# Kernel optimization log

Hardware: AMD Instinct MI355X
Metric: run time of the kernel (lower is better)

Reference implementation:

```python
import jax, jax.numpy as jnp
import numpy as np

B, S, D = 2, 2048, 2048
N_HEADS = 16
HEAD_DIM = D // N_HEADS  # 128


def apply_rotary(xq, xk, cos, sin):
    # xq, xk: [B, S, H, HD]; cos, sin: [S, HD//2]
    def rot(t):
        tr = t.reshape(t.shape[:-1] + (HEAD_DIM // 2, 2))
        r, i = tr[..., 0], tr[..., 1]
        c = cos[None, :, None, :]  # [1, S, 1, HD//2]
        s = sin[None, :, None, :]
        out_r = r * c - i * s
        out_i = r * s + i * c
        return jnp.stack([out_r, out_i], axis=-1).reshape(t.shape)
    return rot(xq), rot(xk)


def setup_inputs() -> dict:
    key = jax.random.key(0)
    k1, k2, k3 = jax.random.split(key, 3)
    x = jax.random.normal(k1, (B, S, D), dtype=jnp.float32)
    wqkv = jax.random.normal(k2, (3 * D, D), dtype=jnp.float32) * (D ** -0.5)
    wo = jax.random.normal(k3, (D, D), dtype=jnp.float32) * (D ** -0.5)
    # rotary tables, standard llama theta=10000
    inv_freq = 1.0 / (10000.0 ** (jnp.arange(0, HEAD_DIM, 2, dtype=jnp.float32) / HEAD_DIM))
    t = jnp.arange(S, dtype=jnp.float32)
    freqs = jnp.outer(t, inv_freq)  # [S, HD//2]
    freqs_cos = jnp.cos(freqs)
    freqs_sin = jnp.sin(freqs)
    # causal additive mask [1, 1, S, S]
    causal = jnp.tril(jnp.ones((S, S), dtype=bool))
    mask = jnp.where(causal, 0.0, -jnp.inf).astype(jnp.float32)[None, None]
    return {"x": x, "freqs_cos": freqs_cos, "freqs_sin": freqs_sin,
            "mask": mask, "wqkv": wqkv, "wo": wo, "input_pos": 0}


def reference(x, freqs_cos, freqs_sin, mask, wqkv, wo, input_pos):
    # fused QKV projection (Linear: x @ W^T)
    qkv = jnp.einsum('bsd,ed->bse', x, wqkv)  # [B, S, 3D]
    xq, xk, xv = jnp.split(qkv, 3, axis=-1)
    xq = xq.reshape(B, S, N_HEADS, HEAD_DIM)
    xk = xk.reshape(B, S, N_HEADS, HEAD_DIM)
    xv = xv.reshape(B, S, N_HEADS, HEAD_DIM)
    xq, xk = apply_rotary(xq, xk, freqs_cos, freqs_sin)
    # SDPA (kv_cache is None; input_pos unused)
    scale = HEAD_DIM ** -0.5
    scores = jnp.einsum('bqhd,bkhd->bhqk', xq, xk) * scale + mask
    attn = jax.nn.softmax(scores, axis=-1)
    out = jnp.einsum('bhqk,bkhd->bqhd', attn, xv).reshape(B, S, D)
    return jnp.einsum('bsd,ed->bse', out, wo)
```

## Files before the change

### kernel.cpp

```cpp
#include <hip/hip_runtime.h>

#define B_ 2
#define S_ 2048
#define D_ 2048
#define H_ 16
#define DH_ 128
#define E3_ (3*D_)

#define AS1 __attribute__((address_space(1)))
#define AS3 __attribute__((address_space(3)))

typedef __attribute__((ext_vector_type(4))) float f32x4;
typedef __attribute__((ext_vector_type(8))) short bf16x8;

__device__ __forceinline__ unsigned short f2bf(float f) {
  unsigned u = __float_as_uint(f);
  u += 0x7fff + ((u >> 16) & 1);
  return (unsigned short)(u >> 16);
}
__device__ __forceinline__ float bf2f(unsigned short h) {
  return __uint_as_float(((unsigned)h) << 16);
}
__device__ __forceinline__ unsigned cvt_pk_bf16(float lo, float hi) {
  unsigned r;
  asm("v_cvt_pk_bf16_f32 %0, %1, %2" : "=v"(r) : "v"(lo), "v"(hi));
  return r;
}

__global__ void cast_f32_bf16(const float* __restrict__ in, unsigned short* __restrict__ out, int n4) {
  int i = blockIdx.x * 256 + threadIdx.x;
  if (i >= n4) return;
  float4 v = reinterpret_cast<const float4*>(in)[i];
  ushort4 o;
  o.x = f2bf(v.x); o.y = f2bf(v.y); o.z = f2bf(v.z); o.w = f2bf(v.w);
  reinterpret_cast<ushort4*>(out)[i] = o;
}

__global__ __launch_bounds__(512) void gemm_qkv256(const unsigned short* __restrict__ A,
                                                   const unsigned short* __restrict__ Bm,
                                                   unsigned short* __restrict__ qkv,
                                                   unsigned short* __restrict__ Vt) {
  __shared__ __align__(16) unsigned short As[2][256*64];
  __shared__ __align__(16) unsigned short Bs[2][192*64];
  const int t = threadIdx.x;
  const int lane = t & 63;
  const int w = t >> 6;
  const int wr = w >> 2, wc = w & 3;
  const int l16 = lane & 15, lg = lane >> 4;
  const int bm = blockIdx.y, bn = blockIdx.x;

  f32x4 acc[8][3] = {};

#define STG1(KT)                                                                                   \
  {                                                                                                \
    const int k0s = (KT) * 64;                                                                     \
    const int bufs = (KT) & 1;                                                                     \
    _Pragma("unroll")                                                                              \
    for (int rr = 0; rr < 4; ++rr) {                                                               \
      int e = t*8 + rr*4096;                                                                       \
      int row = e >> 6, g = (e >> 3) & 7, gs = g ^ (row & 7);                                      \
      const unsigned short* ga = A + (size_t)(bm*256 + row)*2048 + k0s + gs*8;                     \
      __builtin_amdgcn_global_load_lds((const AS1 unsigned int*)ga,                                \
                                       (AS3 unsigned int*)(&As[bufs][e]), 16, 0, 0);               \
    }                                                                                              \
    _Pragma("unroll")                                                                              \
    for (int rr = 0; rr < 3; ++rr) {                                                               \
      int e = t*8 + rr*4096;                                                                       \
      int row = e >> 6, g = (e >> 3) & 7, gs = g ^ (row & 7);                                      \
      const unsigned short* gb = Bm + (size_t)(bn*192 + row)*2048 + k0s + gs*8;                    \
      __builtin_amdgcn_global_load_lds((const AS1 unsigned int*)gb,                                \
                                       (AS3 unsigned int*)(&Bs[bufs][e]), 16, 0, 0);               \
    }                                                                                              \
  }

  STG1(0);
  STG1(1);

  for (int kt = 0; kt < 32; ++kt) {
    if (kt == 31) { asm volatile("s_waitcnt vmcnt(0)" ::: "memory"); }
    else         { asm volatile("s_waitcnt vmcnt(7)" ::: "memory"); }
    __builtin_amdgcn_s_barrier();
    __builtin_amdgcn_sched_barrier(0);
    const int buf = kt & 1;
#pragma unroll
    for (int kk = 0; kk < 2; ++kk) {
      bf16x8 bfr[3];
#pragma unroll
      for (int ni = 0; ni < 3; ++ni) {
        int row = wc*48 + ni*16 + l16;
        int g = kk*4 + lg;
        bfr[ni] = *reinterpret_cast<const bf16x8*>(&Bs[buf][row*64 + ((g ^ (row & 7))<<3)]);
      }
#pragma unroll
      for (int mh = 0; mh < 2; ++mh) {
        bf16x8 afr[4];
#pragma unroll
        for (int m4 = 0; m4 < 4; ++m4) {
          int row = wr*128 + (mh*4 + m4)*16 + l16;
          int g = kk*4 + lg;
          afr[m4] = *reinterpret_cast<const bf16x8*>(&As[buf][row*64 + ((g ^ (row & 7))<<3)]);
        }
#pragma unroll
        for (int m4 = 0; m4 < 4; ++m4)
#pragma unroll
          for (int ni = 0; ni < 3; ++ni)
            acc[mh*4 + m4][ni] = __builtin_amdgcn_mfma_f32_16x16x32_bf16(afr[m4], bfr[ni], acc[mh*4 + m4][ni], 0, 0, 0);
      }
    }
    __builtin_amdgcn_s_barrier();
    if (kt < 30) STG1(kt + 2);
  }
#undef STG1

#pragma unroll
  for (int mi = 0; mi < 8; ++mi) {
#pragma unroll
    for (int ni = 0; ni < 3; ++ni) {
      int col = bn*192 + wc*48 + ni*16 + l16;
      int row0 = bm*256 + wr*128 + mi*16 + lg*4;
      if (col < 4096) {
#pragma unroll
        for (int r = 0; r < 4; ++r)
          qkv[(size_t)(row0 + r)*4096 + col] = f2bf(acc[mi][ni][r]);
      } else {
        int colv = col - 4096;
        int h = colv >> 7, d = colv & 127;
        int b = row0 >> 11, s = row0 & 2047;
        ushort4 v4;
        v4.x = f2bf(acc[mi][ni][0]);
        v4.y = f2bf(acc[mi][ni][1]);
        v4.z = f2bf(acc[mi][ni][2]);
        v4.w = f2bf(acc[mi][ni][3]);
        *reinterpret_cast<ushort4*>(&Vt[(((size_t)(b*H_ + h))*DH_ + d)*S_ + s]) = v4;
      }
    }
  }
}

__global__ __launch_bounds__(256) void gemm_bt(const unsigned short* __restrict__ A,
                                               const unsigned short* __restrict__ Bm,
                                               float* __restrict__ C,
                                               int Ndim, int Kdim) {
  __shared__ __align__(16) unsigned short As[128*64];
  __shared__ __align__(16) unsigned short Bs[128*64];
  const int t = threadIdx.x;
  const int lane = t & 63;
  const int w = t >> 6;
  const int wm = w >> 1, wn = w & 1;
  const int l16 = lane & 15, lg = lane >> 4;
  const int bm = blockIdx.y, bn = blockIdx.x;

  f32x4 acc[4][4] = {};
  const int e0 = t * 8;

  for (int k0 = 0; k0 < Kdim; k0 += 64) {
#pragma unroll
    for (int it = 0; it < 4; ++it) {
      int e = e0 + it * 2048;
      int row = e >> 6;
      int g = (e >> 3) & 7;
      int gs = g ^ (row & 7);
      const unsigned short* ga = A  + (size_t)(bm*128 + row) * Kdim + k0 + gs*8;
      const unsigned short* gb = Bm + (size_t)(bn*128 + row) * Kdim + k0 + gs*8;
      __builtin_amdgcn_global_load_lds((const AS1 unsigned int*)ga,
                                       (AS3 unsigned int*)(&As[e]), 16, 0, 0);
      __builtin_amdgcn_global_load_lds((const AS1 unsigned int*)gb,
                                       (AS3 unsigned int*)(&Bs[e]), 16, 0, 0);
    }
    __syncthreads();
#pragma unroll
    for (int kk = 0; kk < 2; ++kk) {
      bf16x8 a[4], b[4];
#pragma unroll
      for (int mi = 0; mi < 4; ++mi) {
        int row = wm*64 + mi*16 + l16;
        int gw = kk*4 + lg;
        a[mi] = *reinterpret_cast<const bf16x8*>(&As[row*64 + ((gw ^ (row & 7))<<3)]);
      }
#pragma unroll
      for (int ni = 0; ni < 4; ++ni) {
        int row = wn*64 + ni*16 + l16;
        int gw = kk*4 + lg;
        b[ni] = *reinterpret_cast<const bf16x8*>(&Bs[row*64 + ((gw ^ (row & 7))<<3)]);
      }
#pragma unroll
      for (int mi = 0; mi < 4; ++mi)
#pragma unroll
        for (int ni = 0; ni < 4; ++ni)
          acc[mi][ni] = __builtin_amdgcn_mfma_f32_16x16x32_bf16(a[mi], b[ni], acc[mi][ni], 0, 0, 0);
    }
    __syncthreads();
  }
#pragma unroll
  for (int mi = 0; mi < 4; ++mi) {
#pragma unroll
    for (int ni = 0; ni < 4; ++ni) {
      int col = bn*128 + wn*64 + ni*16 + l16;
      int row0 = bm*128 + wm*64 + mi*16 + lg*4;
#pragma unroll
      for (int r = 0; r < 4; ++r)
        C[(size_t)(row0 + r) * Ndim + col] = acc[mi][ni][r];
    }
  }
}

__global__ __launch_bounds__(256) void rope_qk(const unsigned short* __restrict__ qkv,
                                               const float* __restrict__ cosT,
                                               const float* __restrict__ sinT,
                                               unsigned short* __restrict__ Q,
                                               unsigned short* __restrict__ K) {
  const float SCLQ = 0.08838834764831845f * 1.4426950408889634f;
  const int idx = blockIdx.x;
  const int b = idx >> 11, s = idx & 2047;
  const int t = threadIdx.x;
  const int e = t * 8;
  const int h = e >> 7, d0 = e & 127;
  const int j0 = d0 >> 1;
  const size_t rowb = (size_t)(b*S_ + s) * 4096;
  float4 c4 = *reinterpret_cast<const float4*>(&cosT[s*64 + j0]);
  float4 s4 = *reinterpret_cast<const float4*>(&sinT[s*64 + j0]);
  float cc[4] = {c4.x, c4.y, c4.z, c4.w};
  float ss[4] = {s4.x, s4.y, s4.z, s4.w};
  const size_t qo = (((size_t)(b*H_ + h)) * S_ + s) * DH_ + d0;

  ushort4 qv[2], kv[2], qd[2], kd[2];
  qv[0] = *reinterpret_cast<const ushort4*>(&qkv[rowb + e]);
  qv[1] = *reinterpret_cast<const ushort4*>(&qkv[rowb + e + 4]);
  kv[0] = *reinterpret_cast<const ushort4*>(&qkv[rowb + 2048 + e]);
  kv[1] = *reinterpret_cast<const ushort4*>(&qkv[rowb + 2048 + e + 4]);
#pragma unroll
  for (int p = 0; p < 4; ++p) {
    unsigned short* qi = (unsigned short*)&qv[p >> 1] + (p & 1) * 2;
    unsigned short* ki = (unsigned short*)&kv[p >> 1] + (p & 1) * 2;
    unsigned short* qo2 = (unsigned short*)&qd[p >> 1] + (p & 1) * 2;
    unsigned short* ko2 = (unsigned short*)&kd[p >> 1] + (p & 1) * 2;
    float x0 = bf2f(qi[0]), x1 = bf2f(qi[1]);
    qo2[0] = f2bf((x0*cc[p] - x1*ss[p]) * SCLQ);
    qo2[1] = f2bf((x0*ss[p] + x1*cc[p]) * SCLQ);
    float y0 = bf2f(ki[0]), y1 = bf2f(ki[1]);
    ko2[0] = f2bf(y0*cc[p] - y1*ss[p]);
    ko2[1] = f2bf(y0*ss[p] + y1*cc[p]);
  }
  *reinterpret_cast<ushort4*>(&Q[qo])     = qd[0];
  *reinterpret_cast<ushort4*>(&Q[qo + 4]) = qd[1];
  *reinterpret_cast<ushort4*>(&K[qo])     = kd[0];
  *reinterpret_cast<ushort4*>(&K[qo + 4]) = kd[1];
}

#define NQT 32
__global__ __launch_bounds__(512) void attn(const unsigned short* __restrict__ Q,
                                            const unsigned short* __restrict__ K,
                                            const unsigned short* __restrict__ Vt,
                                            unsigned short* __restrict__ O) {
  __shared__ __align__(16) unsigned short Ks[2][64*128];
  __shared__ __align__(16) unsigned short Vs[2][128*64];
  __shared__ __align__(16) unsigned short Plds[8][16*64];
  const int orig = blockIdx.y * gridDim.x + blockIdx.x;
  const int wgid = (orig & 7) * 64 + (orig >> 3);
  const int x = wgid & 15;
  const int bh = wgid >> 4;
  const int b = bh >> 4, h = bh & 15;
  const int t = threadIdx.x;
  const int lane = t & 63;
  const int w = t >> 6;
  const int wg8 = w >> 2;
  const int wi = w & 3;
  const int l16 = lane & 15, lg = lane >> 4;
  const int qt = wg8 ? (NQT - 1 - x) : x;
  const int q0 = qt * 64 + wi * 16;
  const unsigned short* Qh = Q  + (size_t)bh * S_ * DH_;
  const unsigned short* Kh = K  + (size_t)bh * S_ * DH_;
  const unsigned short* Vh = Vt + (size_t)bh * DH_ * S_;

  bf16x8 aq[4];
#pragma unroll
  for (int kk = 0; kk < 4; ++kk)
    aq[kk] = *reinterpret_cast<const bf16x8*>(Qh + (size_t)(q0 + l16)*DH_ + kk*32 + lg*8);

  f32x4 o[8] = {};
  float mrun = -1e30f, lrun = 0.f;
  const int ntiles = NQT - x;

#define STAGE_KV(TILE)                                                                              \
  {                                                                                                 \
    const int kv0s = (TILE) * 64;                                                                   \
    unsigned short* Kd = &Ks[(TILE) & 1][0];                                                        \
    unsigned short* Vd = &Vs[(TILE) & 1][0];                                                        \
    _Pragma("unroll")                                                                               \
    for (int it = 0; it < 2; ++it) {                                                                \
      int e = t*8 + it*4096;                                                                        \
      int row = e >> 7;                                                                             \
      int gslot = (e >> 3) & 15;                                                                    \
      int gsrc = gslot ^ (row & 7);                                                                 \
      const unsigned short* ga = Kh + (size_t)(kv0s + row) * DH_ + gsrc*8;                          \
      __builtin_amdgcn_global_load_lds((const AS1 unsigned int*)ga,                                 \
                                       (AS3 unsigned int*)(&Kd[e]), 16, 0, 0);                      \
    }                                                                                               \
    _Pragma("unroll")                                                                               \
    for (int it = 0; it < 2; ++it) {                                                                \
      int e = t*8 + it*4096;                                                                        \
      int dd = e >> 6;                                                                              \
      int gslot = (e >> 3) & 7;                                                                     \
      int gsrc = gslot ^ (dd & 7);                                                                  \
      const unsigned short* gv = Vh + (size_t)dd * S_ + kv0s + gsrc*8;                              \
      __builtin_amdgcn_global_load_lds((const AS1 unsigned int*)gv,                                 \
                                       (AS3 unsigned int*)(&Vd[e]), 16, 0, 0);                      \
    }                                                                                               \
  }

  STAGE_KV(0);

  for (int tile = 0; tile < ntiles; ++tile) {
    __syncthreads();
    if (tile + 1 < ntiles) STAGE_KV(tile + 1);
    const int kv0 = tile * 64;
    const int buf = tile & 1;

    if (tile <= qt) {
      f32x4 sc[4] = {};
      __builtin_amdgcn_s_setprio(1);
#pragma unroll
      for (int kk = 0; kk < 4; ++kk) {
#pragma unroll
        for (int n = 0; n < 4; ++n) {
          int row = n*16 + l16;
          int g = kk*4 + lg;
          bf16x8 bk = *reinterpret_cast<const bf16x8*>(&Ks[buf][row*128 + ((g ^ (row & 7))<<3)]);
          sc[n] = __builtin_amdgcn_mfma_f32_16x16x32_bf16(bk, aq[kk], sc[n], 0, 0, 0);
        }
      }
      __builtin_amdgcn_s_setprio(0);
      if (tile == qt) {
        int qrow = q0 + l16;
#pragma unroll
        for (int n = 0; n < 4; ++n)
#pragma unroll
          for (int r = 0; r < 4; ++r) {
            int kidx = kv0 + n*16 + lg*4 + r;
            sc[n][r] = (kidx > qrow) ? -1e30f : sc[n][r];
          }
      }
      float mt = sc[0][0];
#pragma unroll
      for (int n = 0; n < 4; ++n)
#pragma unroll
        for (int r = 0; r < 4; ++r) mt = fmaxf(mt, sc[n][r]);
      mt = fmaxf(mt, __shfl_xor(mt, 16));
      mt = fmaxf(mt, __shfl_xor(mt, 32));
      if (__any(mt > mrun + 8.f)) {
        float mnew = fmaxf(mrun, mt);
        float alpha = __builtin_amdgcn_exp2f(mrun - mnew);
        mrun = mnew;
        lrun *= alpha;
        float ar[4];
#pragma unroll
        for (int r = 0; r < 4; ++r) ar[r] = __shfl(alpha, lg*4 + r);
#pragma unroll
        for (int n2 = 0; n2 < 8; ++n2)
#pragma unroll
          for (int r = 0; r < 4; ++r) o[n2][r] *= ar[r];
      }
      float rs = 0.f;
      unsigned pk[4][2];
#pragma unroll
      for (int n = 0; n < 4; ++n) {
        float p0 = __builtin_amdgcn_exp2f(sc[n][0] - mrun);
        float p1 = __builtin_amdgcn_exp2f(sc[n][1] - mrun);
        float p2 = __builtin_amdgcn_exp2f(sc[n][2] - mrun);
        float p3 = __builtin_amdgcn_exp2f(sc[n][3] - mrun);
        rs += (p0 + p1) + (p2 + p3);
        pk[n][0] = cvt_pk_bf16(p0, p1);
        pk[n][1] = cvt_pk_bf16(p2, p3);
      }
      rs += __shfl_xor(rs, 16);
      rs += __shfl_xor(rs, 32);
      lrun += rs;
      unsigned short* Pw = &Plds[w][0];
      char* Pb = (char*)Pw + l16*128;
#pragma unroll
      for (int n = 0; n < 4; ++n) {
        int sslot = (n*4 + lg) ^ (l16 & 14);
        *reinterpret_cast<uint2*>(Pb + sslot*8) = make_uint2(pk[n][0], pk[n][1]);
      }
      bf16x8 pa[2];
#pragma unroll
      for (int kk2 = 0; kk2 < 2; ++kk2) {
        int tp = (kk2*4 + lg) ^ ((l16 >> 1) & 7);
        pa[kk2] = *reinterpret_cast<const bf16x8*>(Pb + tp*16);
      }
      __builtin_amdgcn_s_setprio(1);
#pragma unroll
      for (int kk2 = 0; kk2 < 2; ++kk2) {
#pragma unroll
        for (int n2 = 0; n2 < 8; ++n2) {
          int d = n2*16 + l16;
          int g = kk2*4 + lg;
          bf16x8 bv = *reinterpret_cast<const bf16x8*>(&Vs[buf][d*64 + ((g ^ (d & 7))<<3)]);
          o[n2] = __builtin_amdgcn_mfma_f32_16x16x32_bf16(pa[kk2], bv, o[n2], 0, 0, 0);
        }
      }
      __builtin_amdgcn_s_setprio(0);
    }
  }
  float linv = 1.f / lrun;
  float lr[4];
#pragma unroll
  for (int r = 0; r < 4; ++r) lr[r] = __shfl(linv, lg*4 + r);
  size_t ob = ((size_t)b * S_) * D_;
#pragma unroll
  for (int n2 = 0; n2 < 8; ++n2) {
#pragma unroll
    for (int r = 0; r < 4; ++r) {
      int rowq = q0 + lg*4 + r;
      int d = n2*16 + l16;
      O[ob + (size_t)rowq * D_ + h*DH_ + d] = f2bf(o[n2][r] * lr[r]);
    }
  }
}

extern "C" void kernel_launch(void* const* d_in, const int* in_sizes, int n_in,
                              void* d_out, int out_size, void* d_ws, size_t ws_size,
                              hipStream_t stream) {
  const float* x    = (const float*)d_in[0];
  const float* fcos = (const float*)d_in[1];
  const float* fsin = (const float*)d_in[2];
  const float* wqkv = (const float*)d_in[4];
  const float* wo   = (const float*)d_in[5];
  float* out = (float*)d_out;
  char* ws = (char*)d_ws;

  unsigned short* xb    = (unsigned short*)(ws);
  unsigned short* wqkvb = (unsigned short*)(ws + 16777216);
  unsigned short* wob   = (unsigned short*)(ws + 41943040);
  unsigned short* qkv   = (unsigned short*)(ws + 50331648);
  unsigned short* Qb    = (unsigned short*)(ws + 83886080);
  unsigned short* Kb    = (unsigned short*)(ws + 100663296);
  unsigned short* Vtb   = (unsigned short*)(ws + 117440512);
  unsigned short* attn_out = xb;

  cast_f32_bf16<<<dim3(2097152/256), 256, 0, stream>>>(x, xb, 2097152);
  cast_f32_bf16<<<dim3(3145728/256), 256, 0, stream>>>(wqkv, wqkvb, 3145728);
  cast_f32_bf16<<<dim3(1048576/256), 256, 0, stream>>>(wo, wob, 1048576);

  gemm_qkv256<<<dim3(32, 16), 512, 0, stream>>>(xb, wqkvb, qkv, Vtb);
  rope_qk<<<dim3(4096), 256, 0, stream>>>(qkv, fcos, fsin, Qb, Kb);
  attn<<<dim3(16, 32), 512, 0, stream>>>(Qb, Kb, Vtb, attn_out);
  gemm_bt<<<dim3(16, 32), 256, 0, stream>>>(attn_out, wob, out, 2048, 2048);
}
```

Measured before the change: 248.4 us.

## Double-buffer output GEMM, restructure QKV GEMM LDS reads, merge cast kernels

Merges the three fp32→bf16 cast launches into one kernel that picks its source by global index, removing two launches. Restructures the QKV GEMM inner loop so both k-halves of the fragments are read from LDS up front, with MFMA issue interleaved around the barrier and next-stage prefetch and wrapped in s_setprio. Converts the output-projection GEMM from single-buffered LDS with full syncthreads to a double-buffered global_load_lds pipeline with the same split-phase schedule. This doubles LDS use in gemm_bt and raises register pressure from holding both fragment halves, which may lower occupancy.

```diff
diff --git a/kernel.cpp b/kernel.cpp
--- a/kernel.cpp
+++ b/kernel.cpp
@@ -5,7 +5,6 @@
 #define D_ 2048
 #define H_ 16
 #define DH_ 128
-#define E3_ (3*D_)
 
 #define AS1 __attribute__((address_space(1)))
 #define AS3 __attribute__((address_space(3)))
@@ -27,13 +26,21 @@
   return r;
 }
 
-__global__ void cast_f32_bf16(const float* __restrict__ in, unsigned short* __restrict__ out, int n4) {
+__global__ __launch_bounds__(256) void cast3(const float* __restrict__ x,
+                                             const float* __restrict__ wq,
+                                             const float* __restrict__ wo,
+                                             unsigned short* __restrict__ xb,
+                                             unsigned short* __restrict__ wqb,
+                                             unsigned short* __restrict__ wob) {
   int i = blockIdx.x * 256 + threadIdx.x;
-  if (i >= n4) return;
-  float4 v = reinterpret_cast<const float4*>(in)[i];
+  const float* src; unsigned short* dst; int off;
+  if (i < 2097152)      { src = x;  dst = xb;  off = i; }
+  else if (i < 5242880) { src = wq; dst = wqb; off = i - 2097152; }
+  else                  { src = wo; dst = wob; off = i - 5242880; }
+  float4 v = reinterpret_cast<const float4*>(src)[off];
   ushort4 o;
   o.x = f2bf(v.x); o.y = f2bf(v.y); o.z = f2bf(v.z); o.w = f2bf(v.w);
-  reinterpret_cast<ushort4*>(out)[i] = o;
+  reinterpret_cast<ushort4*>(dst)[off] = o;
 }
 
 __global__ __launch_bounds__(512) void gemm_qkv256(const unsigned short* __restrict__ A,
@@ -77,38 +84,56 @@
   STG1(1);
 
   for (int kt = 0; kt < 32; ++kt) {
+    const int buf = kt & 1;
     if (kt == 31) { asm volatile("s_waitcnt vmcnt(0)" ::: "memory"); }
-    else         { asm volatile("s_waitcnt vmcnt(7)" ::: "memory"); }
+    else          { asm volatile("s_waitcnt vmcnt(7)" ::: "memory"); }
     __builtin_amdgcn_s_barrier();
     __builtin_amdgcn_sched_barrier(0);
-    const int buf = kt & 1;
-#pragma unroll
-    for (int kk = 0; kk < 2; ++kk) {
-      bf16x8 bfr[3];
-#pragma unroll
-      for (int ni = 0; ni < 3; ++ni) {
-        int row = wc*48 + ni*16 + l16;
-        int g = kk*4 + lg;
-        bfr[ni] = *reinterpret_cast<const bf16x8*>(&Bs[buf][row*64 + ((g ^ (row & 7))<<3)]);
-      }
-#pragma unroll
-      for (int mh = 0; mh < 2; ++mh) {
-        bf16x8 afr[4];
-#pragma unroll
-        for (int m4 = 0; m4 < 4; ++m4) {
-          int row = wr*128 + (mh*4 + m4)*16 + l16;
-          int g = kk*4 + lg;
-          afr[m4] = *reinterpret_cast<const bf16x8*>(&As[buf][row*64 + ((g ^ (row & 7))<<3)]);
-        }
-#pragma unroll
-        for (int m4 = 0; m4 < 4; ++m4)
-#pragma unroll
-          for (int ni = 0; ni < 3; ++ni)
-            acc[mh*4 + m4][ni] = __builtin_amdgcn_mfma_f32_16x16x32_bf16(afr[m4], bfr[ni], acc[mh*4 + m4][ni], 0, 0, 0);
-      }
-    }
+    bf16x8 a0[8], b0[3];
+#pragma unroll
+    for (int ni = 0; ni < 3; ++ni) {
+      int row = wc*48 + ni*16 + l16;
+      b0[ni] = *reinterpret_cast<const bf16x8*>(&Bs[buf][row*64 + ((lg ^ (row & 7))<<3)]);
+    }
+#pragma unroll
+    for (int m8 = 0; m8 < 8; ++m8) {
+      int row = wr*128 + m8*16 + l16;
+      a0[m8] = *reinterpret_cast<const bf16x8*>(&As[buf][row*64 + ((lg ^ (row & 7))<<3)]);
+    }
+    asm volatile("s_waitcnt lgkmcnt(0)" ::: "memory");
+    __builtin_amdgcn_sched_barrier(0);
+    bf16x8 a1[8], b1[3];
+#pragma unroll
+    for (int ni = 0; ni < 3; ++ni) {
+      int row = wc*48 + ni*16 + l16;
+      int g = 4 + lg;
+      b1[ni] = *reinterpret_cast<const bf16x8*>(&Bs[buf][row*64 + ((g ^ (row & 7))<<3)]);
+    }
+#pragma unroll
+    for (int m8 = 0; m8 < 8; ++m8) {
+      int row = wr*128 + m8*16 + l16;
+      int g = 4 + lg;
+      a1[m8] = *reinterpret_cast<const bf16x8*>(&As[buf][row*64 + ((g ^ (row & 7))<<3)]);
+    }
+    __builtin_amdgcn_sched_barrier(0);
+    __builtin_amdgcn_s_setprio(1);
+#pragma unroll
+    for (int m8 = 0; m8 < 8; ++m8)
+#pragma unroll
+      for (int ni = 0; ni < 3; ++ni)
+        acc[m8][ni] = __builtin_amdgcn_mfma_f32_16x16x32_bf16(a0[m8], b0[ni], acc[m8][ni], 0, 0, 0);
+    __builtin_amdgcn_s_setprio(0);
+    asm volatile("s_waitcnt lgkmcnt(0)" ::: "memory");
+    __builtin_amdgcn_sched_barrier(0);
     __builtin_amdgcn_s_barrier();
     if (kt < 30) STG1(kt + 2);
+    __builtin_amdgcn_s_setprio(1);
+#pragma unroll
+    for (int m8 = 0; m8 < 8; ++m8)
+#pragma unroll
+      for (int ni = 0; ni < 3; ++ni)
+        acc[m8][ni] = __builtin_amdgcn_mfma_f32_16x16x32_bf16(a1[m8], b1[ni], acc[m8][ni], 0, 0, 0);
+    __builtin_amdgcn_s_setprio(0);
   }
 #undef STG1
 
@@ -141,56 +166,85 @@
                                                const unsigned short* __restrict__ Bm,
                                                float* __restrict__ C,
                                                int Ndim, int Kdim) {
-  __shared__ __align__(16) unsigned short As[128*64];
-  __shared__ __align__(16) unsigned short Bs[128*64];
+  __shared__ __align__(16) unsigned short As[2][128*64];
+  __shared__ __align__(16) unsigned short Bs[2][128*64];
   const int t = threadIdx.x;
   const int lane = t & 63;
   const int w = t >> 6;
   const int wm = w >> 1, wn = w & 1;
   const int l16 = lane & 15, lg = lane >> 4;
   const int bm = blockIdx.y, bn = blockIdx.x;
+  const int nkt = Kdim >> 6;
 
   f32x4 acc[4][4] = {};
-  const int e0 = t * 8;
-
-  for (int k0 = 0; k0 < Kdim; k0 += 64) {
-#pragma unroll
-    for (int it = 0; it < 4; ++it) {
-      int e = e0 + it * 2048;
-      int row = e >> 6;
-      int g = (e >> 3) & 7;
-      int gs = g ^ (row & 7);
-      const unsigned short* ga = A  + (size_t)(bm*128 + row) * Kdim + k0 + gs*8;
-      const unsigned short* gb = Bm + (size_t)(bn*128 + row) * Kdim + k0 + gs*8;
-      __builtin_amdgcn_global_load_lds((const AS1 unsigned int*)ga,
-                                       (AS3 unsigned int*)(&As[e]), 16, 0, 0);
-      __builtin_amdgcn_global_load_lds((const AS1 unsigned int*)gb,
-                                       (AS3 unsigned int*)(&Bs[e]), 16, 0, 0);
-    }
-    __syncthreads();
-#pragma unroll
-    for (int kk = 0; kk < 2; ++kk) {
-      bf16x8 a[4], b[4];
-#pragma unroll
-      for (int mi = 0; mi < 4; ++mi) {
-        int row = wm*64 + mi*16 + l16;
-        int gw = kk*4 + lg;
-        a[mi] = *reinterpret_cast<const bf16x8*>(&As[row*64 + ((gw ^ (row & 7))<<3)]);
-      }
-#pragma unroll
-      for (int ni = 0; ni < 4; ++ni) {
-        int row = wn*64 + ni*16 + l16;
-        int gw = kk*4 + lg;
-        b[ni] = *reinterpret_cast<const bf16x8*>(&Bs[row*64 + ((gw ^ (row & 7))<<3)]);
-      }
-#pragma unroll
-      for (int mi = 0; mi < 4; ++mi)
-#pragma unroll
-        for (int ni = 0; ni < 4; ++ni)
-          acc[mi][ni] = __builtin_amdgcn_mfma_f32_16x16x32_bf16(a[mi], b[ni], acc[mi][ni], 0, 0, 0);
-    }
-    __syncthreads();
-  }
+
+#define STG2(KT)                                                                                   \
+  {                                                                                                \
+    const int k0s = (KT) * 64;                                                                     \
+    const int bufs = (KT) & 1;                                                                     \
+    _Pragma("unroll")                                                                              \
+    for (int it = 0; it < 4; ++it) {                                                               \
+      int e = t*8 + it*2048;                                                                       \
+      int row = e >> 6, g = (e >> 3) & 7, gs = g ^ (row & 7);                                      \
+      const unsigned short* ga = A  + (size_t)(bm*128 + row)*Kdim + k0s + gs*8;                    \
+      const unsigned short* gb = Bm + (size_t)(bn*128 + row)*Kdim + k0s + gs*8;                    \
+      __builtin_amdgcn_global_load_lds((const AS1 unsigned int*)ga,                                \
+                                       (AS3 unsigned int*)(&As[bufs][e]), 16, 0, 0);               \
+      __builtin_amdgcn_global_load_lds((const AS1 unsigned int*)gb,                                \
+                                       (AS3 unsigned int*)(&Bs[bufs][e]), 16, 0, 0);               \
+    }                                                                                              \
+  }
+
+  STG2(0);
+  STG2(1);
+
+  for (int kt = 0; kt < nkt; ++kt) {
+    const int buf = kt & 1;
+    if (kt == nkt - 1) { asm volatile("s_waitcnt vmcnt(0)" ::: "memory"); }
+    else               { asm volatile("s_waitcnt vmcnt(8)" ::: "memory"); }
+    __builtin_amdgcn_s_barrier();
+    __builtin_amdgcn_sched_barrier(0);
+    bf16x8 a0[4], b0[4];
+#pragma unroll
+    for (int mi = 0; mi < 4; ++mi) {
+      int rowa = wm*64 + mi*16 + l16;
+      a0[mi] = *reinterpret_cast<const bf16x8*>(&As[buf][rowa*64 + ((lg ^ (rowa & 7))<<3)]);
+      int rowb = wn*64 + mi*16 + l16;
+      b0[mi] = *reinterpret_cast<const bf16x8*>(&Bs[buf][rowb*64 + ((lg ^ (rowb & 7))<<3)]);
+    }
+    asm volatile("s_waitcnt lgkmcnt(0)" ::: "memory");
+    __builtin_amdgcn_sched_barrier(0);
+    bf16x8 a1[4], b1[4];
+#pragma unroll
+    for (int mi = 0; mi < 4; ++mi) {
+      int g = 4 + lg;
+      int rowa = wm*64 + mi*16 + l16;
+      a1[mi] = *reinterpret_cast<const bf16x8*>(&As[buf][rowa*64 + ((g ^ (rowa & 7))<<3)]);
+      int rowb = wn*64 + mi*16 + l16;
+      b1[mi] = *reinterpret_cast<const bf16x8*>(&Bs[buf][rowb*64 + ((g ^ (rowb & 7))<<3)]);
+    }
+    __builtin_amdgcn_sched_barrier(0);
+    __builtin_amdgcn_s_setprio(1);
+#pragma unroll
+    for (int mi = 0; mi < 4; ++mi)
+#pragma unroll
+      for (int ni = 0; ni < 4; ++ni)
+        acc[mi][ni] = __builtin_amdgcn_mfma_f32_16x16x32_bf16(a0[mi], b0[ni], acc[mi][ni], 0, 0, 0);
+    __builtin_amdgcn_s_setprio(0);
+    asm volatile("s_waitcnt lgkmcnt(0)" ::: "memory");
+    __builtin_amdgcn_sched_barrier(0);
+    __builtin_amdgcn_s_barrier();
+    if (kt < nkt - 2) STG2(kt + 2);
+    __builtin_amdgcn_s_setprio(1);
+#pragma unroll
+    for (int mi = 0; mi < 4; ++mi)
+#pragma unroll
+      for (int ni = 0; ni < 4; ++ni)
+        acc[mi][ni] = __builtin_amdgcn_mfma_f32_16x16x32_bf16(a1[mi], b1[ni], acc[mi][ni], 0, 0, 0);
+    __builtin_amdgcn_s_setprio(0);
+  }
+#undef STG2
+
 #pragma unroll
   for (int mi = 0; mi < 4; ++mi) {
 #pragma unroll
@@ -438,9 +492,7 @@
   unsigned short* Vtb   = (unsigned short*)(ws + 117440512);
   unsigned short* attn_out = xb;
 
-  cast_f32_bf16<<<dim3(2097152/256), 256, 0, stream>>>(x, xb, 2097152);
-  cast_f32_bf16<<<dim3(3145728/256), 256, 0, stream>>>(wqkv, wqkvb, 3145728);
-  cast_f32_bf16<<<dim3(1048576/256), 256, 0, stream>>>(wo, wob, 1048576);
+  cast3<<<dim3(24576), 256, 0, stream>>>(x, wqkv, wo, xb, wqkvb, wob);
 
   gemm_qkv256<<<dim3(32, 16), 512, 0, stream>>>(xb, wqkvb, qkv, Vtb);
   rope_qk<<<dim3(4096), 256, 0, stream>>>(qkv, fcos, fsin, Qb, Kb);
```

After: 232.0 us. 6.6% less time.
